# Optimization experiments

Hardware: AMD Instinct MI355X
Metric: run time of the kernel (lower is better)

Reference implementation:

```python
import jax, jax.numpy as jnp
import numpy as np

B, N = 16, 4096

def _fps(xyz, npoint):
    # iterative farthest point sampling on one cloud [n,3] -> [npoint] int32
    n = xyz.shape[0]
    def body(carry, _):
        dist, far = carry
        d = jnp.sum((xyz - xyz[far]) ** 2, axis=-1)
        dist = jnp.minimum(dist, d)
        return (dist, jnp.argmax(dist).astype(jnp.int32)), far
    _, idx = jax.lax.scan(body, (jnp.full((n,), 1e10, jnp.float32), jnp.int32(0)), None, length=npoint)
    return idx

def _ball_query(radius, nsample, xyz, new_xyz):
    # xyz [n,3], new_xyz [S,3] -> [S,nsample] neighbor indices (first-in-index order, as in PointNet++)
    n = xyz.shape[0]
    sqr = jnp.sum((new_xyz[:, None, :] - xyz[None, :, :]) ** 2, axis=-1)  # [S,n]
    idx = jnp.where(sqr > radius * radius, n, jnp.arange(n, dtype=jnp.int32)[None, :])
    idx = jnp.sort(idx, axis=-1)[:, :nsample]
    return jnp.where(idx == n, idx[:, :1], idx)

def _gather(p, i):
    return jax.vmap(lambda pp, ii: pp[ii])(p, i)

def _mlp(x, layers):
    # shared MLP = 1x1 conv over grouped points; BN(eval) folded into (W,b)
    for W, b in layers:
        x = jax.nn.relu(jnp.einsum('bsnc,co->bsno', x, W) + b)
    return x

def _sa(xyz, feats, npoint, radius, nsample, layers):
    fps_idx = jax.vmap(lambda p: _fps(p, npoint))(xyz)            # [B,S]
    new_xyz = _gather(xyz, fps_idx)                                # [B,S,3]
    idx = jax.vmap(lambda p, q: _ball_query(radius, nsample, p, q))(xyz, new_xyz)  # [B,S,ns]
    x = _gather(xyz, idx) - new_xyz[:, :, None, :]                 # centered grouped xyz
    if feats is not None:
        x = jnp.concatenate([x, _gather(feats, idx)], axis=-1)
    x = _mlp(x, layers)
    return new_xyz, jnp.max(x, axis=2)

def _forward(points, w10, b10, w11, b11, w12, b12, w20, b20, w21, b21, w22, b22, w30, b30, w31, b31, w32, b32, lw1, lb1, lw2, lb2, fw1, fb1, fw2, fb2, pos_mean, pos_std, rot_mean, rot_std):
    l1x, l1f = _sa(points, None, 512, 0.2, 32, [(w10, b10), (w11, b11), (w12, b12)])
    l2x, l2f = _sa(l1x, l1f, 128, 0.4, 64, [(w20, b20), (w21, b21), (w22, b22)])
    # sa3: group_all
    x = jnp.concatenate([l2x, l2f], axis=-1)[:, None]              # [B,1,128,259]
    x = _mlp(x, [(w30, b30), (w31, b31), (w32, b32)])
    g = jnp.max(x, axis=2).reshape(points.shape[0], 1024)
    label = jax.nn.sigmoid(jax.nn.relu(g @ lw1 + lb1) @ lw2 + lb2)  # dropout = identity (eval)
    res = jax.nn.relu(g @ fw1 + fb1) @ fw2 + fb2
    pl = res[:, 0:3] * pos_std + pos_mean
    rl = res[:, 3:9] * rot_std + rot_mean
    pr = res[:, 9:12] * pos_std + pos_mean
    rr = res[:, 12:18] * rot_std + rot_mean
    return jnp.concatenate([label, pl, rl, pr, rr], axis=-1)       # [B,20]

def setup_inputs():
    ks = iter(jax.random.split(jax.random.key(0), 64))
    def w(shape, s=0.05):
        return jax.random.normal(next(ks), shape, jnp.float32) * s
    inp = {'points': jax.random.normal(next(ks), (B, N, 3), jnp.float32) * 0.5}
    dims = {'w10': (3, 64), 'w11': (64, 64), 'w12': (64, 128), 'w20': (131, 128), 'w21': (128, 128), 'w22': (128, 256), 'w30': (259, 256), 'w31': (256, 512), 'w32': (512, 1024), 'lw1': (1024, 256), 'lw2': (256, 2), 'fw1': (1024, 512), 'fw2': (512, 18)}
    for name, s in dims.items():
        inp[name] = w(s)
        inp[name.replace('w', 'b', 1)] = jnp.zeros((s[1],), jnp.float32)
    inp['pos_mean'] = w((3,), 0.1)
    inp['pos_std'] = jnp.abs(w((3,))) + 1.0
    inp['rot_mean'] = w((6,), 0.1)
    inp['rot_std'] = jnp.abs(w((6,))) + 1.0
    return inp

def reference(points, w10, b10, w11, b11, w12, b12, w20, b20, w21, b21, w22, b22, w30, b30, w31, b31, w32, b32, lw1, lb1, lw2, lb2, fw1, fb1, fw2, fb2, pos_mean, pos_std, rot_mean, rot_std):
    return _forward(points, w10, b10, w11, b11, w12, b12, w20, b20, w21, b21, w22, b22, w30, b30, w31, b31, w32, b32, lw1, lb1, lw2, lb2, fw1, fb1, fw2, fb2, pos_mean, pos_std, rot_mean, rot_std)
```

## Files before the change

kernel.cpp:

```cpp
#include <hip/hip_runtime.h>
#include <math.h>

#define BB 16
#define NN 4096

typedef float v2f __attribute__((ext_vector_type(2)));
typedef short bfrag8 __attribute__((ext_vector_type(8)));
typedef float fx4 __attribute__((ext_vector_type(4)));

__device__ __forceinline__ v2f pkfma(v2f a, v2f b, v2f c) {
    return __builtin_elementwise_fma(a, b, c);
}

__device__ __forceinline__ fx4 mfma16(bfrag8 a, bfrag8 b, fx4 c) {
    return __builtin_amdgcn_mfma_f32_16x16x32_bf16(a, b, c, 0, 0, 0);
}

__device__ __forceinline__ unsigned short bf16rne(float v) {
    unsigned u = __float_as_uint(v);
    return (unsigned short)((u + 0x7FFFu + ((u >> 16) & 1u)) >> 16);
}
__device__ __forceinline__ void bf16split(float v, unsigned short& h, unsigned short& l) {
    h = bf16rne(v);
    float fh = __uint_as_float((unsigned)h << 16);
    l = bf16rne(v - fh);
}

__device__ __forceinline__ float sq3(float dx, float dy, float dz) {
    return __fadd_rn(__fadd_rn(__fmul_rn(dx, dx), __fmul_rn(dy, dy)), __fmul_rn(dz, dz));
}

template<int CTRL, int RMASK>
__device__ __forceinline__ unsigned long long dpp_max_step(unsigned long long P) {
    int lo = __builtin_amdgcn_update_dpp(0, (int)(unsigned)P,        CTRL, RMASK, 0xf, true);
    int hi = __builtin_amdgcn_update_dpp(0, (int)(unsigned)(P >> 32), CTRL, RMASK, 0xf, true);
    unsigned long long o = ((unsigned long long)(unsigned)hi << 32) | (unsigned)lo;
    return (o > P) ? o : P;
}

__device__ __forceinline__ unsigned long long dpp_wave_max_u64(unsigned long long P) {
    P = dpp_max_step<0x111, 0xf>(P);
    P = dpp_max_step<0x112, 0xf>(P);
    P = dpp_max_step<0x114, 0xf>(P);
    P = dpp_max_step<0x118, 0xf>(P);
    P = dpp_max_step<0x142, 0xa>(P);
    P = dpp_max_step<0x143, 0xc>(P);
    return P;
}

__device__ __forceinline__ unsigned long long u64max(unsigned long long a, unsigned long long b) {
    return (a > b) ? a : b;
}

template<int NPTS, int NPOINT, int TPB>
__global__ __launch_bounds__(TPB) void fps_kernel(const float* __restrict__ xyz,
                                                  float* __restrict__ newxyz,
                                                  float* __restrict__ out_t,
                                                  int ts) {
    constexpr int PPT = NPTS / TPB;
    constexpr int NW  = TPB / 64;
    static_assert(NPOINT <= TPB, "far-history latch needs NPOINT <= TPB");
    __shared__ float sx[NPTS], sy[NPTS], sz[NPTS];
    __shared__ __align__(16) unsigned long long slot[2][NW];
    const int b = blockIdx.x;
    const int tid = threadIdx.x;
    const float* base = xyz + (size_t)b * NPTS * 3;
    for (int i = tid; i < NPTS; i += TPB) {
        sx[i] = base[i * 3 + 0];
        sy[i] = base[i * 3 + 1];
        sz[i] = base[i * 3 + 2];
    }
    __syncthreads();
    float px[PPT], py[PPT], pz[PPT], dist[PPT];
#pragma unroll
    for (int k = 0; k < PPT; k++) {
        int p = tid + k * TPB;
        px[k] = sx[p]; py[k] = sy[p]; pz[k] = sz[p];
        dist[k] = 1e10f;
    }
    int far = 0;
    int myfar = 0;
    const int lane = tid & 63, wid = tid >> 6;
    for (int it = 0; it < NPOINT; it++) {
        if (tid == it) myfar = far;
        float fx = sx[far], fy = sy[far], fz = sz[far];
        float bv = -1.0f; int bi = 0;
#pragma unroll
        for (int k = 0; k < PPT; k++) {
            float d = sq3(px[k] - fx, py[k] - fy, pz[k] - fz);
            float nd = fminf(dist[k], d);
            dist[k] = nd;
            if (nd > bv) { bv = nd; bi = tid + k * TPB; }
        }
        unsigned long long P = ((unsigned long long)__float_as_uint(bv) << 32)
                             | (unsigned long long)(~(unsigned)bi & 0xFFFFFFFFull);
        P = dpp_wave_max_u64(P);
        int bufi = it & 1;
        if (lane == 63) slot[bufi][wid] = P;
        __syncthreads();
        unsigned long long v[NW];
#pragma unroll
        for (int w = 0; w < NW; w++) v[w] = slot[bufi][w];
#pragma unroll
        for (int st = NW / 2; st >= 1; st >>= 1)
#pragma unroll
            for (int w = 0; w < st; w++) v[w] = u64max(v[w], v[w + st]);
        far = (int)(~(unsigned)(v[0] & 0xFFFFFFFFull));
    }
    if (tid < NPOINT) {
        float fx = sx[myfar], fy = sy[myfar], fz = sz[myfar];
        newxyz[((size_t)b * NPOINT + tid) * 3 + 0] = fx;
        newxyz[((size_t)b * NPOINT + tid) * 3 + 1] = fy;
        newxyz[((size_t)b * NPOINT + tid) * 3 + 2] = fz;
        if (out_t) {
            out_t[0 * ts + b * NPOINT + tid] = fx;
            out_t[1 * ts + b * NPOINT + tid] = fy;
            out_t[2 * ts + b * NPOINT + tid] = fz;
        }
    }
}

template<int NS>
__device__ __forceinline__ void bq_body(const float* __restrict__ pts, int n,
                                        const float* __restrict__ centers, int S,
                                        float r2, int* __restrict__ outidx,
                                        int wave, int lane) {
    int b = wave / S, s = wave % S;
    const float* c = centers + ((size_t)b * S + s) * 3;
    float cx = c[0], cy = c[1], cz = c[2];
    const float* pb = pts + (size_t)b * n * 3;
    int* out = outidx + ((size_t)b * S + s) * NS;
    int total = 0, first = -1;
    int rounds = n >> 6;
    for (int r = 0; r < rounds; r++) {
        int p = (r << 6) + lane;
        float dx = pb[p * 3 + 0] - cx, dy = pb[p * 3 + 1] - cy, dz = pb[p * 3 + 2] - cz;
        float d = sq3(dx, dy, dz);
        bool pred = (d <= r2);
        unsigned long long mask = __ballot(pred);
        if (first < 0 && mask) first = (r << 6) + (__ffsll(mask) - 1);
        if (pred) {
            int rank = total + __popcll(mask & ((1ull << lane) - 1ull));
            if (rank < NS) out[rank] = p;
        }
        total += __popcll(mask);
        if (total >= NS) break;
    }
    for (int j = total + lane; j < NS; j += 64) out[j] = first;
}

__global__ __launch_bounds__(512) void bq1_fps2_kernel(const float* __restrict__ points,
                                                       const float* __restrict__ l1x,
                                                       float* __restrict__ l2x,
                                                       float* __restrict__ x3t,
                                                       int* __restrict__ idx1,
                                                       float r2a,
                                                       const float* __restrict__ w21,
                                                       const float* __restrict__ w22,
                                                       const float* __restrict__ w11s,
                                                       const float* __restrict__ w12s,
                                                       const float* __restrict__ w20s,
                                                       float* __restrict__ w21f,
                                                       float* __restrict__ w22f,
                                                       float* __restrict__ w11f,
                                                       float* __restrict__ w12f,
                                                       float* __restrict__ w20f) {
    __shared__ float sx[512], sy[512], sz[512];
    const int tid = threadIdx.x;
    const int lane = tid & 63, wid = tid >> 6;
    if (blockIdx.x < 16) {
        if (wid != 0) return;
        const int b = blockIdx.x;
        const float* base = l1x + (size_t)b * 512 * 3;
        for (int i = lane; i < 512; i += 64) {
            sx[i] = base[i * 3 + 0];
            sy[i] = base[i * 3 + 1];
            sz[i] = base[i * 3 + 2];
        }
        float px[8], py[8], pz[8], dist[8];
#pragma unroll
        for (int k = 0; k < 8; k++) {
            int p = lane + k * 64;
            px[k] = sx[p]; py[k] = sy[p]; pz[k] = sz[p];
            dist[k] = 1e10f;
        }
        int far = 0, myfar0 = 0, myfar1 = 0;
        for (int it = 0; it < 128; it++) {
            if (lane == it) myfar0 = far;
            if (lane == it - 64) myfar1 = far;
            float fx = sx[far], fy = sy[far], fz = sz[far];
            float bv = -1.0f; int bi = 0;
#pragma unroll
            for (int k = 0; k < 8; k++) {
                float d = sq3(px[k] - fx, py[k] - fy, pz[k] - fz);
                float nd = fminf(dist[k], d);
                dist[k] = nd;
                if (nd > bv) { bv = nd; bi = lane + k * 64; }
            }
            unsigned long long P = ((unsigned long long)__float_as_uint(bv) << 32)
                                 | (unsigned long long)(~(unsigned)bi & 0xFFFFFFFFull);
            P = dpp_wave_max_u64(P);
            unsigned lo = (unsigned)__builtin_amdgcn_readlane((int)(unsigned)P, 63);
            far = (int)(~lo);
        }
        {
            int s0 = lane, s1 = lane + 64;
            float a = sx[myfar0], c1 = sy[myfar0], c2 = sz[myfar0];
            l2x[((size_t)b * 128 + s0) * 3 + 0] = a;
            l2x[((size_t)b * 128 + s0) * 3 + 1] = c1;
            l2x[((size_t)b * 128 + s0) * 3 + 2] = c2;
            x3t[0 * 2048 + b * 128 + s0] = a;
            x3t[1 * 2048 + b * 128 + s0] = c1;
            x3t[2 * 2048 + b * 128 + s0] = c2;
            float d = sx[myfar1], e = sy[myfar1], f = sz[myfar1];
            l2x[((size_t)b * 128 + s1) * 3 + 0] = d;
            l2x[((size_t)b * 128 + s1) * 3 + 1] = e;
            l2x[((size_t)b * 128 + s1) * 3 + 2] = f;
            x3t[0 * 2048 + b * 128 + s1] = d;
            x3t[1 * 2048 + b * 128 + s1] = e;
            x3t[2 * 2048 + b * 128 + s1] = f;
        }
    } else if (blockIdx.x < 1040) {
        int wave = (blockIdx.x - 16) * 8 + wid;
        bq_body<32>(points, 4096, l1x, 512, r2a, idx1, wave, lane);
    } else {
        int gt = (blockIdx.x - 1040) * 512 + tid;
        const float* W; float* OF; int NT, KT, N; int t;
        if (gt < 4096)       { W = w21;        OF = w21f; NT = 8;  KT = 4; N = 128; t = gt; }
        else if (gt < 12288) { W = w22;        OF = w22f; NT = 16; KT = 4; N = 256; t = gt - 4096; }
        else if (gt < 13312) { W = w11s;       OF = w11f; NT = 4;  KT = 2; N = 64;  t = gt - 12288; }
        else if (gt < 15360) { W = w12s;       OF = w12f; NT = 8;  KT = 2; N = 128; t = gt - 13312; }
        else                 { W = w20s + 384; OF = w20f; NT = 8;  KT = 4; N = 128; t = gt - 15360; }
        int L = t & 63;
        int rest = t >> 6;
        int nt = rest & (NT - 1);
        int hk = rest / NT;
        int kt = hk % KT, hl = hk / KT;
        int k0 = kt * 32 + (L >> 4) * 8;
        int n  = nt * 16 + (L & 15);
        unsigned o[4];
#pragma unroll
        for (int e = 0; e < 4; e++) {
            float va = W[(size_t)(k0 + 2 * e + 0) * N + n];
            float vb = W[(size_t)(k0 + 2 * e + 1) * N + n];
            unsigned short ha, la, hb, lb;
            bf16split(va, ha, la);
            bf16split(vb, hb, lb);
            o[e] = hl ? ((unsigned)la | ((unsigned)lb << 16))
                      : ((unsigned)ha | ((unsigned)hb << 16));
        }
        ((uint4*)OF)[t] = make_uint4(o[0], o[1], o[2], o[3]);
    }
}

__global__ __launch_bounds__(64, 2) void sa1_bq2_kernel(const float* __restrict__ xyz, const float* __restrict__ l1x,
                                                 const int* __restrict__ idx1,
                                                 const float* __restrict__ l2x, int* __restrict__ idx2, float r2b,
                                                 const float* __restrict__ W1, const float* __restrict__ B1,
                                                 const float* __restrict__ W2f, const float* __restrict__ B2,
                                                 const float* __restrict__ W3f, const float* __restrict__ B3,
                                                 float* __restrict__ l1f) {
    __shared__ short hsh[64 * 72];
    __shared__ short hsl[64 * 72];
    int lane = threadIdx.x;
    if (blockIdx.x < 2048) {
        bq_body<64>(l1x, 512, l2x, 128, r2b, idx2, blockIdx.x, lane);
        return;
    }
    int blk = blockIdx.x - 2048;
    int b = blk >> 8;
    int ct = lane >> 5, nn = lane & 31;
    int s = ((blk & 255) << 1) | ct;
    int center = b * 512 + s;
    int c0 = b * 512 + ((blk & 255) << 1);
    int ii = idx1[center * 32 + nn];
    float px = xyz[((size_t)b * NN + ii) * 3 + 0] - l1x[(size_t)center * 3 + 0];
    float py = xyz[((size_t)b * NN + ii) * 3 + 1] - l1x[(size_t)center * 3 + 1];
    float pz = xyz[((size_t)b * NN + ii) * 3 + 2] - l1x[(size_t)center * 3 + 2];
#pragma unroll
    for (int c2 = 0; c2 < 32; c2++) {
        int ca = 2 * c2, cb = 2 * c2 + 1;
        float v0 = fmaxf(B1[ca] + px * W1[ca] + py * W1[64 + ca] + pz * W1[128 + ca], 0.0f);
        float v1 = fmaxf(B1[cb] + px * W1[cb] + py * W1[64 + cb] + pz * W1[128 + cb], 0.0f);
        unsigned short h0, l0, h1, l1;
        bf16split(v0, h0, l0);
        bf16split(v1, h1, l1);
        int base = lane * 72 + ca;
        *(unsigned*)(&hsh[base]) = (unsigned)h0 | ((unsigned)h1 << 16);
        *(unsigned*)(&hsl[base]) = (unsigned)l0 | ((unsigned)l1 << 16);
    }
    __syncthreads();
    {
        fx4 acc[4][4];
#pragma unroll
        for (int mt = 0; mt < 4; mt++)
#pragma unroll
            for (int nt = 0; nt < 4; nt++) {
                float bn = B2[nt * 16 + (lane & 15)];
                acc[mt][nt] = (fx4){bn, bn, bn, bn};
            }
        const bfrag8* w2v = (const bfrag8*)W2f;
#pragma unroll
        for (int kt = 0; kt < 2; kt++) {
            bfrag8 ah[4], al[4];
#pragma unroll
            for (int mt = 0; mt < 4; mt++) {
                int idx = (mt * 16 + (lane & 15)) * 72 + kt * 32 + (lane >> 4) * 8;
                ah[mt] = *(const bfrag8*)(&hsh[idx]);
                al[mt] = *(const bfrag8*)(&hsl[idx]);
            }
#pragma unroll
            for (int nt = 0; nt < 4; nt++) {
                bfrag8 bh = w2v[(size_t)((0 + kt) * 4 + nt) * 64 + lane];
                bfrag8 bl = w2v[(size_t)((2 + kt) * 4 + nt) * 64 + lane];
#pragma unroll
                for (int mt = 0; mt < 4; mt++) {
                    acc[mt][nt] = mfma16(ah[mt], bh, acc[mt][nt]);
                    acc[mt][nt] = mfma16(ah[mt], bl, acc[mt][nt]);
                    acc[mt][nt] = mfma16(al[mt], bh, acc[mt][nt]);
                }
            }
        }
        __syncthreads();
#pragma unroll
        for (int mt = 0; mt < 4; mt++)
#pragma unroll
            for (int nt = 0; nt < 4; nt++)
#pragma unroll
                for (int r = 0; r < 4; r++) {
                    float v = fmaxf(acc[mt][nt][r], 0.0f);
                    int m = mt * 16 + (lane >> 4) * 4 + r;
                    int n = nt * 16 + (lane & 15);
                    unsigned short hb, lb;
                    bf16split(v, hb, lb);
                    hsh[m * 72 + n] = (short)hb;
                    hsl[m * 72 + n] = (short)lb;
                }
        __syncthreads();
    }
    const bfrag8* w3v = (const bfrag8*)W3f;
#pragma unroll 1
    for (int pass = 0; pass < 2; pass++) {
        int nbase = pass * 4;
        fx4 acc[4][4];
#pragma unroll
        for (int mt = 0; mt < 4; mt++)
#pragma unroll
            for (int nt = 0; nt < 4; nt++) {
                float bn = B3[(nbase + nt) * 16 + (lane & 15)];
                acc[mt][nt] = (fx4){bn, bn, bn, bn};
            }
#pragma unroll
        for (int kt = 0; kt < 2; kt++) {
            bfrag8 ah[4], al[4];
#pragma unroll
            for (int mt = 0; mt < 4; mt++) {
                int idx = (mt * 16 + (lane & 15)) * 72 + kt * 32 + (lane >> 4) * 8;
                ah[mt] = *(const bfrag8*)(&hsh[idx]);
                al[mt] = *(const bfrag8*)(&hsl[idx]);
            }
#pragma unroll
            for (int nt = 0; nt < 4; nt++) {
                bfrag8 bh = w3v[(size_t)((0 + kt) * 8 + nbase + nt) * 64 + lane];
                bfrag8 bl = w3v[(size_t)((2 + kt) * 8 + nbase + nt) * 64 + lane];
#pragma unroll
                for (int mt = 0; mt < 4; mt++) {
                    acc[mt][nt] = mfma16(ah[mt], bh, acc[mt][nt]);
                    acc[mt][nt] = mfma16(ah[mt], bl, acc[mt][nt]);
                    acc[mt][nt] = mfma16(al[mt], bh, acc[mt][nt]);
                }
            }
        }
#pragma unroll
        for (int nt = 0; nt < 4; nt++) {
            float mv0 = 0.0f, mv1 = 0.0f;
#pragma unroll
            for (int r = 0; r < 4; r++) {
                mv0 = fmaxf(mv0, fmaxf(acc[0][nt][r], acc[1][nt][r]));
                mv1 = fmaxf(mv1, fmaxf(acc[2][nt][r], acc[3][nt][r]));
            }
            mv0 = fmaxf(mv0, __shfl_xor(mv0, 16));
            mv0 = fmaxf(mv0, __shfl_xor(mv0, 32));
            mv1 = fmaxf(mv1, __shfl_xor(mv1, 16));
            mv1 = fmaxf(mv1, __shfl_xor(mv1, 32));
            int n = (nbase + nt) * 16 + (lane & 15);
            if (lane < 16)      l1f[(size_t)c0 * 128 + n] = mv0;
            else if (lane < 32) l1f[(size_t)(c0 + 1) * 128 + n] = mv1;
        }
    }
}

__global__ __launch_bounds__(256, 4) void sa2_kernel(const float* __restrict__ l1x, const float* __restrict__ l2x,
                                                  const float* __restrict__ l1f, const int* __restrict__ idx2,
                                                  const float* __restrict__ W1, const float* __restrict__ B1,
                                                  const float* __restrict__ w20f,
                                                  const float* __restrict__ w21f, const float* __restrict__ B2,
                                                  const float* __restrict__ w22f, const float* __restrict__ B3,
                                                  float* __restrict__ x3t) {
    __shared__ short hsh[64 * 136];
    __shared__ short hsl[64 * 136];
    __shared__ float sxyz[64 * 4];
    int tid = threadIdx.x;
    int w = __builtin_amdgcn_readfirstlane(tid >> 6);
    int lane = tid & 63;
    int b = blockIdx.x >> 7, s = blockIdx.x & 127;
    int center = b * 128 + s;
    int ii = idx2[center * 64 + lane];
    float cx = l2x[(size_t)center * 3 + 0], cy = l2x[(size_t)center * 3 + 1], cz = l2x[(size_t)center * 3 + 2];
    const float* pr = l1x + ((size_t)b * 512 + ii) * 3;
    float px = pr[0] - cx, py = pr[1] - cy, pz = pr[2] - cz;
    if (w == 0) {
        sxyz[lane * 4 + 0] = px;
        sxyz[lane * 4 + 1] = py;
        sxyz[lane * 4 + 2] = pz;
    }
    {
        const float4* frow = (const float4*)(l1f + ((size_t)b * 512 + ii) * 128);
#pragma unroll
        for (int j = 0; j < 8; j++) {
            float4 f = frow[w * 8 + j];
            unsigned short h0, l0, h1, l1, h2, l2, h3, l3;
            bf16split(f.x, h0, l0);
            bf16split(f.y, h1, l1);
            bf16split(f.z, h2, l2);
            bf16split(f.w, h3, l3);
            int cb = lane * 136 + w * 32 + 4 * j;
            *(unsigned*)(&hsh[cb + 0]) = (unsigned)h0 | ((unsigned)h1 << 16);
            *(unsigned*)(&hsh[cb + 2]) = (unsigned)h2 | ((unsigned)h3 << 16);
            *(unsigned*)(&hsl[cb + 0]) = (unsigned)l0 | ((unsigned)l1 << 16);
            *(unsigned*)(&hsl[cb + 2]) = (unsigned)l2 | ((unsigned)l3 << 16);
        }
    }
    __syncthreads();
    {
        fx4 acc[4][2];
        float w0n[2], w1n[2], w2n[2];
#pragma unroll
        for (int nt = 0; nt < 2; nt++) {
            int n = (2 * w + nt) * 16 + (lane & 15);
            float bn = B1[n];
            acc[0][nt] = (fx4){bn, bn, bn, bn};
            acc[1][nt] = acc[0][nt]; acc[2][nt] = acc[0][nt]; acc[3][nt] = acc[0][nt];
            w0n[nt] = W1[n]; w1n[nt] = W1[128 + n]; w2n[nt] = W1[256 + n];
        }
#pragma unroll
        for (int mt = 0; mt < 4; mt++)
#pragma unroll
            for (int r = 0; r < 4; r++) {
                int m = mt * 16 + (lane >> 4) * 4 + r;
                float mx = sxyz[m * 4 + 0], my = sxyz[m * 4 + 1], mz = sxyz[m * 4 + 2];
#pragma unroll
                for (int nt = 0; nt < 2; nt++)
                    acc[mt][nt][r] += mx * w0n[nt] + my * w1n[nt] + mz * w2n[nt];
            }
#pragma unroll
        for (int kt = 0; kt < 4; kt++) {
            bfrag8 ah[4], al[4];
#pragma unroll
            for (int mt = 0; mt < 4; mt++) {
                int idx = (mt * 16 + (lane & 15)) * 136 + kt * 32 + (lane >> 4) * 8;
                ah[mt] = *(const bfrag8*)(&hsh[idx]);
                al[mt] = *(const bfrag8*)(&hsl[idx]);
            }
#pragma unroll
            for (int nt = 0; nt < 2; nt++) {
                int ng = 2 * w + nt;
                bfrag8 bh = ((const bfrag8*)w20f)[(size_t)((0 + kt) * 8 + ng) * 64 + lane];
                bfrag8 bl = ((const bfrag8*)w20f)[(size_t)((4 + kt) * 8 + ng) * 64 + lane];
#pragma unroll
                for (int mt = 0; mt < 4; mt++) {
                    acc[mt][nt] = mfma16(ah[mt], bh, acc[mt][nt]);
                    acc[mt][nt] = mfma16(ah[mt], bl, acc[mt][nt]);
                    acc[mt][nt] = mfma16(al[mt], bh, acc[mt][nt]);
                }
            }
        }
        __syncthreads();
#pragma unroll
        for (int mt = 0; mt < 4; mt++)
#pragma unroll
            for (int nt = 0; nt < 2; nt++)
#pragma unroll
                for (int r = 0; r < 4; r++) {
                    float v = fmaxf(acc[mt][nt][r], 0.0f);
                    int m = mt * 16 + (lane >> 4) * 4 + r;
                    int n = (2 * w + nt) * 16 + (lane & 15);
                    unsigned short hb, lb;
                    bf16split(v, hb, lb);
                    hsh[m * 136 + n] = (short)hb;
                    hsl[m * 136 + n] = (short)lb;
                }
        __syncthreads();
    }
    {
        fx4 acc[4][2];
#pragma unroll
        for (int mt = 0; mt < 4; mt++)
#pragma unroll
            for (int nt = 0; nt < 2; nt++) {
                float bn = B2[(2 * w + nt) * 16 + (lane & 15)];
                acc[mt][nt] = (fx4){bn, bn, bn, bn};
            }
#pragma unroll
        for (int kt = 0; kt < 4; kt++) {
            bfrag8 ah[4], al[4];
#pragma unroll
            for (int mt = 0; mt < 4; mt++) {
                int idx = (mt * 16 + (lane & 15)) * 136 + kt * 32 + (lane >> 4) * 8;
                ah[mt] = *(const bfrag8*)(&hsh[idx]);
                al[mt] = *(const bfrag8*)(&hsl[idx]);
            }
#pragma unroll
            for (int nt = 0; nt < 2; nt++) {
                int ng = 2 * w + nt;
                bfrag8 bh = ((const bfrag8*)w21f)[(size_t)((0 + kt) * 8 + ng) * 64 + lane];
                bfrag8 bl = ((const bfrag8*)w21f)[(size_t)((4 + kt) * 8 + ng) * 64 + lane];
#pragma unroll
                for (int mt = 0; mt < 4; mt++) {
                    acc[mt][nt] = mfma16(ah[mt], bh, acc[mt][nt]);
                    acc[mt][nt] = mfma16(ah[mt], bl, acc[mt][nt]);
                    acc[mt][nt] = mfma16(al[mt], bh, acc[mt][nt]);
                }
            }
        }
        __syncthreads();
#pragma unroll
        for (int mt = 0; mt < 4; mt++)
#pragma unroll
            for (int nt = 0; nt < 2; nt++)
#pragma unroll
                for (int r = 0; r < 4; r++) {
                    float v = fmaxf(acc[mt][nt][r], 0.0f);
                    int m = mt * 16 + (lane >> 4) * 4 + r;
                    int n = (2 * w + nt) * 16 + (lane & 15);
                    unsigned short hb, lb;
                    bf16split(v, hb, lb);
                    hsh[m * 136 + n] = (short)hb;
                    hsl[m * 136 + n] = (short)lb;
                }
        __syncthreads();
    }
#pragma unroll 1
    for (int pass = 0; pass < 2; pass++) {
        int nb = w * 4 + pass * 2;
        fx4 acc[4][2];
#pragma unroll
        for (int mt = 0; mt < 4; mt++)
#pragma unroll
            for (int nt = 0; nt < 2; nt++) {
                float bn = B3[(nb + nt) * 16 + (lane & 15)];
                acc[mt][nt] = (fx4){bn, bn, bn, bn};
            }
#pragma unroll
        for (int kt = 0; kt < 4; kt++) {
            bfrag8 ah[4], al[4];
#pragma unroll
            for (int mt = 0; mt < 4; mt++) {
                int idx = (mt * 16 + (lane & 15)) * 136 + kt * 32 + (lane >> 4) * 8;
                ah[mt] = *(const bfrag8*)(&hsh[idx]);
                al[mt] = *(const bfrag8*)(&hsl[idx]);
            }
#pragma unroll
            for (int nt = 0; nt < 2; nt++) {
                bfrag8 bh = ((const bfrag8*)w22f)[(size_t)((0 + kt) * 16 + (nb + nt)) * 64 + lane];
                bfrag8 bl = ((const bfrag8*)w22f)[(size_t)((4 + kt) * 16 + (nb + nt)) * 64 + lane];
#pragma unroll
                for (int mt = 0; mt < 4; mt++) {
                    acc[mt][nt] = mfma16(ah[mt], bh, acc[mt][nt]);
                    acc[mt][nt] = mfma16(ah[mt], bl, acc[mt][nt]);
                    acc[mt][nt] = mfma16(al[mt], bh, acc[mt][nt]);
                }
            }
        }
#pragma unroll
        for (int nt = 0; nt < 2; nt++) {
            float mv = 0.0f;
#pragma unroll
            for (int mt = 0; mt < 4; mt++)
#pragma unroll
                for (int r = 0; r < 4; r++)
                    mv = fmaxf(mv, acc[mt][nt][r]);
            mv = fmaxf(mv, __shfl_xor(mv, 16));
            mv = fmaxf(mv, __shfl_xor(mv, 32));
            if (lane < 16)
                x3t[(size_t)(3 + (nb + nt) * 16 + lane) * 2048 + center] = mv;
        }
    }
}

template<int K, int COUT, int CPT, bool MAXOUT>
__device__ __forceinline__ void gemm_t_body(const float* __restrict__ in_t,
                                            const float* __restrict__ W,
                                            const float* __restrict__ bias,
                                            float* __restrict__ outp,
                                            int bid, int lane) {
    int rw = bid & 31, cg = bid >> 5;
    int row = rw * 64 + lane;
    int cbase = cg * CPT;
    v2f acc[CPT / 2];
    const v2f* bv = (const v2f*)(bias + cbase);
#pragma unroll
    for (int j = 0; j < CPT / 2; j++) acc[j] = bv[j];
    for (int k = 0; k < K; k++) {
        float xk = in_t[(size_t)k * 2048 + row];
        v2f xk2 = {xk, xk};
        const v2f* wr = (const v2f*)(W + (size_t)k * COUT + cbase);
#pragma unroll
        for (int j = 0; j < CPT / 2; j++) acc[j] = pkfma(xk2, wr[j], acc[j]);
    }
    if (MAXOUT) {
        int b = row >> 7;
#pragma unroll
        for (int j = 0; j < CPT / 2; j++) {
            float va = fmaxf(acc[j].x, 0.0f);
            float vb = fmaxf(acc[j].y, 0.0f);
#pragma unroll
            for (int m = 32; m >= 1; m >>= 1) {
                va = fmaxf(va, __shfl_xor(va, m));
                vb = fmaxf(vb, __shfl_xor(vb, m));
            }
            if (lane == 0) {
                atomicMax((int*)(outp + (size_t)b * 1024 + cbase + 2 * j + 0), __float_as_int(va));
                atomicMax((int*)(outp + (size_t)b * 1024 + cbase + 2 * j + 1), __float_as_int(vb));
            }
        }
    } else {
#pragma unroll
        for (int j = 0; j < CPT / 2; j++) {
            outp[(size_t)(cbase + 2 * j + 0) * 2048 + row] = fmaxf(acc[j].x, 0.0f);
            outp[(size_t)(cbase + 2 * j + 1) * 2048 + row] = fmaxf(acc[j].y, 0.0f);
        }
    }
}

template<int K, int COUT, int CPT, bool MAXOUT>
__global__ __launch_bounds__(64, 4) void gemm_t_kernel(const float* __restrict__ in_t,
                                                    const float* __restrict__ W,
                                                    const float* __restrict__ bias,
                                                    float* __restrict__ outp) {
    gemm_t_body<K, COUT, CPT, MAXOUT>(in_t, W, bias, outp, blockIdx.x, threadIdx.x);
}

__global__ __launch_bounds__(64, 4) void gemm1_zerog_kernel(const float* __restrict__ in_t,
                                                            const float* __restrict__ W,
                                                            const float* __restrict__ bias,
                                                            float* __restrict__ outp,
                                                            float* __restrict__ g) {
    if (blockIdx.x < 1024) {
        gemm_t_body<259, 256, 8, false>(in_t, W, bias, outp, blockIdx.x, threadIdx.x);
    } else {
        g[(blockIdx.x - 1024) * 64 + threadIdx.x] = 0.0f;
    }
}

__global__ __launch_bounds__(512) void head_kernel(const float* __restrict__ g,
                                                   const float* __restrict__ lw1, const float* __restrict__ lb1,
                                                   const float* __restrict__ lw2, const float* __restrict__ lb2,
                                                   const float* __restrict__ fw1, const float* __restrict__ fb1,
                                                   const float* __restrict__ fw2, const float* __restrict__ fb2,
                                                   const float* __restrict__ pm, const float* __restrict__ ps,
                                                   const float* __restrict__ rm, const float* __restrict__ rs,
                                                   float* __restrict__ out) {
    __shared__ float gl[1024], a1[256], f1[512];
    int b = blockIdx.x, t = threadIdx.x;
    for (int i = t; i < 1024; i += 512) gl[i] = g[b * 1024 + i];
    __syncthreads();
    {
        float acc = fb1[t];
        for (int k = 0; k < 1024; k++) acc += gl[k] * fw1[k * 512 + t];
        f1[t] = fmaxf(acc, 0.0f);
    }
    if (t < 256) {
        float acc = lb1[t];
        for (int k = 0; k < 1024; k++) acc += gl[k] * lw1[k * 256 + t];
        a1[t] = fmaxf(acc, 0.0f);
    }
    __syncthreads();
    if (t < 2) {
        float z = lb2[t];
        for (int k = 0; k < 256; k++) z += a1[k] * lw2[k * 2 + t];
        out[b * 20 + t] = 1.0f / (1.0f + expf(-z));
    } else if (t < 20) {
        int i = t - 2;
        float z = fb2[i];
        for (int k = 0; k < 512; k++) z += f1[k] * fw2[k * 18 + i];
        float sc, mn;
        if (i < 3)       { sc = ps[i];      mn = pm[i]; }
        else if (i < 9)  { sc = rs[i - 3];  mn = rm[i - 3]; }
        else if (i < 12) { sc = ps[i - 9];  mn = pm[i - 9]; }
        else             { sc = rs[i - 12]; mn = rm[i - 12]; }
        out[b * 20 + t] = z * sc + mn;
    }
}

static inline size_t align256(size_t x) { return (x + 255) & ~(size_t)255; }

extern "C" void kernel_launch(void* const* d_in, const int* in_sizes, int n_in,
                              void* d_out, int out_size, void* d_ws, size_t ws_size,
                              hipStream_t stream) {
    const float* points = (const float*)d_in[0];
    const float* w10 = (const float*)d_in[1];  const float* b10 = (const float*)d_in[2];
    const float* w11 = (const float*)d_in[3];  const float* b11 = (const float*)d_in[4];
    const float* w12 = (const float*)d_in[5];  const float* b12 = (const float*)d_in[6];
    const float* w20 = (const float*)d_in[7];  const float* b20 = (const float*)d_in[8];
    const float* w21 = (const float*)d_in[9];  const float* b21 = (const float*)d_in[10];
    const float* w22 = (const float*)d_in[11]; const float* b22 = (const float*)d_in[12];
    const float* w30 = (const float*)d_in[13]; const float* b30 = (const float*)d_in[14];
    const float* w31 = (const float*)d_in[15]; const float* b31 = (const float*)d_in[16];
    const float* w32 = (const float*)d_in[17]; const float* b32 = (const float*)d_in[18];
    const float* lw1 = (const float*)d_in[19]; const float* lb1 = (const float*)d_in[20];
    const float* lw2 = (const float*)d_in[21]; const float* lb2 = (const float*)d_in[22];
    const float* fw1 = (const float*)d_in[23]; const float* fb1 = (const float*)d_in[24];
    const float* fw2 = (const float*)d_in[25]; const float* fb2 = (const float*)d_in[26];
    const float* pm  = (const float*)d_in[27]; const float* ps  = (const float*)d_in[28];
    const float* rm  = (const float*)d_in[29]; const float* rs  = (const float*)d_in[30];
    float* out = (float*)d_out;

    char* p = (char*)d_ws;
    float* l1x  = (float*)p; p += align256((size_t)BB * 512 * 3 * 4);
    int*   idx1 = (int*)p;   p += align256((size_t)BB * 512 * 32 * 4);
    float* l1f  = (float*)p; p += align256((size_t)BB * 512 * 128 * 4);
    float* l2x  = (float*)p; p += align256((size_t)BB * 128 * 3 * 4);
    int*   idx2 = (int*)p;   p += align256((size_t)BB * 128 * 64 * 4);
    float* x3t  = (float*)p; p += align256((size_t)259 * 2048 * 4);
    float* h1t  = (float*)p; p += align256((size_t)256 * 2048 * 4);
    float* h2t  = (float*)p; p += align256((size_t)512 * 2048 * 4);
    float* g    = (float*)p; p += align256((size_t)BB * 1024 * 4);
    float* w21f = h1t;
    float* w22f = h1t + (size_t)16384;
    float* w11f = h1t + (size_t)49152;
    float* w12f = h1t + (size_t)53248;
    float* w20f = h1t + (size_t)61440;

    const float R2A = (float)(0.2 * 0.2);
    const float R2B = (float)(0.4 * 0.4);

    fps_kernel<4096, 512, 512><<<BB, 512, 0, stream>>>(points, l1x, (float*)nullptr, 0);
    bq1_fps2_kernel<<<1078, 512, 0, stream>>>(points, l1x, l2x, x3t, idx1, R2A,
                                              w21, w22, w11, w12, w20,
                                              w21f, w22f, w11f, w12f, w20f);
    sa1_bq2_kernel<<<6144, 64, 0, stream>>>(points, l1x, idx1, l2x, idx2, R2B,
                                            w10, b10, w11f, b11, w12f, b12, l1f);
    sa2_kernel<<<2048, 256, 0, stream>>>(l1x, l2x, l1f, idx2, w20, b20,
                                         w20f, w21f, b21, w22f, b22, x3t);
    gemm1_zerog_kernel<<<1280, 64, 0, stream>>>(x3t, w30, b30, h1t, g);
    gemm_t_kernel<256, 512, 8, false><<<2048, 64, 0, stream>>>(h1t, w31, b31, h2t);
    gemm_t_kernel<512, 1024, 8, true><<<4096, 64, 0, stream>>>(h2t, w32, b32, g);
    head_kernel<<<BB, 512, 0, stream>>>(g, lw1, lb1, lw2, lb2, fw1, fb1, fw2, fb2, pm, ps, rm, rs, out);
}
```

Measured before the change: 787.3 us.

## Move SA3 MLP layers 2-3 to split-bf16 MFMA GEMMs

Replaces the scalar packed-FMA GEMMs for the 256->512 and 512->1024 SA3 layers with MFMA kernels that emulate fp32 precision using three bf16 products (hi*hi, hi*lo, lo*hi). The first GEMM now writes its activations as hi/lo bf16 pairs in row-major layout, and the extra blocks of that launch pre-split w31/w32 into fragment-ordered buffers that reuse the l1f workspace. This targets the FMA-bound cost of the large SA3 layers. In exchange it adds weight-conversion work on every call and a small precision deviation from dropping the lo*lo term.

Result: faster. 764.0 us, median of 2 (-3.0%).

```diff
diff --git a/kernel.cpp b/kernel.cpp
--- a/kernel.cpp
+++ b/kernel.cpp
@@ -147,6 +147,29 @@
         if (total >= NS) break;
     }
     for (int j = total + lane; j < NS; j += 64) out[j] = first;
+}
+
+__device__ __forceinline__ void wconv_one(const float* __restrict__ W, float* __restrict__ OF,
+                                          int NT, int KT, int N, int t) {
+    int L = t & 63;
+    int rest = t >> 6;
+    int nt = rest & (NT - 1);
+    int hk = rest / NT;
+    int kt = hk % KT, hl = hk / KT;
+    int k0 = kt * 32 + (L >> 4) * 8;
+    int n  = nt * 16 + (L & 15);
+    unsigned o[4];
+#pragma unroll
+    for (int e = 0; e < 4; e++) {
+        float va = W[(size_t)(k0 + 2 * e + 0) * N + n];
+        float vb = W[(size_t)(k0 + 2 * e + 1) * N + n];
+        unsigned short ha, la, hb, lb;
+        bf16split(va, ha, la);
+        bf16split(vb, hb, lb);
+        o[e] = hl ? ((unsigned)la | ((unsigned)lb << 16))
+                  : ((unsigned)ha | ((unsigned)hb << 16));
+    }
+    ((uint4*)OF)[t] = make_uint4(o[0], o[1], o[2], o[3]);
 }
 
 __global__ __launch_bounds__(512) void bq1_fps2_kernel(const float* __restrict__ points,
@@ -225,31 +248,11 @@
         bq_body<32>(points, 4096, l1x, 512, r2a, idx1, wave, lane);
     } else {
         int gt = (blockIdx.x - 1040) * 512 + tid;
-        const float* W; float* OF; int NT, KT, N; int t;
-        if (gt < 4096)       { W = w21;        OF = w21f; NT = 8;  KT = 4; N = 128; t = gt; }
-        else if (gt < 12288) { W = w22;        OF = w22f; NT = 16; KT = 4; N = 256; t = gt - 4096; }
-        else if (gt < 13312) { W = w11s;       OF = w11f; NT = 4;  KT = 2; N = 64;  t = gt - 12288; }
-        else if (gt < 15360) { W = w12s;       OF = w12f; NT = 8;  KT = 2; N = 128; t = gt - 13312; }
-        else                 { W = w20s + 384; OF = w20f; NT = 8;  KT = 4; N = 128; t = gt - 15360; }
-        int L = t & 63;
-        int rest = t >> 6;
-        int nt = rest & (NT - 1);
-        int hk = rest / NT;
-        int kt = hk % KT, hl = hk / KT;
-        int k0 = kt * 32 + (L >> 4) * 8;
-        int n  = nt * 16 + (L & 15);
-        unsigned o[4];
-#pragma unroll
-        for (int e = 0; e < 4; e++) {
-            float va = W[(size_t)(k0 + 2 * e + 0) * N + n];
-            float vb = W[(size_t)(k0 + 2 * e + 1) * N + n];
-            unsigned short ha, la, hb, lb;
-            bf16split(va, ha, la);
-            bf16split(vb, hb, lb);
-            o[e] = hl ? ((unsigned)la | ((unsigned)lb << 16))
-                      : ((unsigned)ha | ((unsigned)hb << 16));
-        }
-        ((uint4*)OF)[t] = make_uint4(o[0], o[1], o[2], o[3]);
+        if (gt < 4096)       wconv_one(w21,        w21f, 8,  4, 128, gt);
+        else if (gt < 12288) wconv_one(w22,        w22f, 16, 4, 256, gt - 4096);
+        else if (gt < 13312) wconv_one(w11s,       w11f, 4,  2, 64,  gt - 12288);
+        else if (gt < 15360) wconv_one(w12s,       w12f, 8,  2, 128, gt - 13312);
+        else                 wconv_one(w20s + 384, w20f, 8,  4, 128, gt - 15360);
     }
 }
 
@@ -588,12 +591,13 @@
     }
 }
 
-template<int K, int COUT, int CPT, bool MAXOUT>
-__device__ __forceinline__ void gemm_t_body(const float* __restrict__ in_t,
-                                            const float* __restrict__ W,
-                                            const float* __restrict__ bias,
-                                            float* __restrict__ outp,
-                                            int bid, int lane) {
+template<int K, int COUT, int CPT>
+__device__ __forceinline__ void gemm1_body_bf16out(const float* __restrict__ in_t,
+                                                   const float* __restrict__ W,
+                                                   const float* __restrict__ bias,
+                                                   unsigned short* __restrict__ oh,
+                                                   unsigned short* __restrict__ ol,
+                                                   int bid, int lane) {
     int rw = bid & 31, cg = bid >> 5;
     int row = rw * 64 + lane;
     int cbase = cg * CPT;
@@ -608,48 +612,117 @@
 #pragma unroll
         for (int j = 0; j < CPT / 2; j++) acc[j] = pkfma(xk2, wr[j], acc[j]);
     }
-    if (MAXOUT) {
-        int b = row >> 7;
-#pragma unroll
-        for (int j = 0; j < CPT / 2; j++) {
-            float va = fmaxf(acc[j].x, 0.0f);
-            float vb = fmaxf(acc[j].y, 0.0f);
-#pragma unroll
-            for (int m = 32; m >= 1; m >>= 1) {
-                va = fmaxf(va, __shfl_xor(va, m));
-                vb = fmaxf(vb, __shfl_xor(vb, m));
-            }
-            if (lane == 0) {
-                atomicMax((int*)(outp + (size_t)b * 1024 + cbase + 2 * j + 0), __float_as_int(va));
-                atomicMax((int*)(outp + (size_t)b * 1024 + cbase + 2 * j + 1), __float_as_int(vb));
-            }
-        }
-    } else {
-#pragma unroll
-        for (int j = 0; j < CPT / 2; j++) {
-            outp[(size_t)(cbase + 2 * j + 0) * 2048 + row] = fmaxf(acc[j].x, 0.0f);
-            outp[(size_t)(cbase + 2 * j + 1) * 2048 + row] = fmaxf(acc[j].y, 0.0f);
-        }
-    }
-}
-
-template<int K, int COUT, int CPT, bool MAXOUT>
-__global__ __launch_bounds__(64, 4) void gemm_t_kernel(const float* __restrict__ in_t,
-                                                    const float* __restrict__ W,
-                                                    const float* __restrict__ bias,
-                                                    float* __restrict__ outp) {
-    gemm_t_body<K, COUT, CPT, MAXOUT>(in_t, W, bias, outp, blockIdx.x, threadIdx.x);
+    unsigned ho[4], lo[4];
+#pragma unroll
+    for (int j = 0; j < CPT / 2; j++) {
+        float va = fmaxf(acc[j].x, 0.0f);
+        float vb = fmaxf(acc[j].y, 0.0f);
+        unsigned short ha, la, hb, lb;
+        bf16split(va, ha, la);
+        bf16split(vb, hb, lb);
+        ho[j] = (unsigned)ha | ((unsigned)hb << 16);
+        lo[j] = (unsigned)la | ((unsigned)lb << 16);
+    }
+    size_t idx = ((size_t)row * COUT + cbase) >> 3;
+    ((uint4*)oh)[idx] = make_uint4(ho[0], ho[1], ho[2], ho[3]);
+    ((uint4*)ol)[idx] = make_uint4(lo[0], lo[1], lo[2], lo[3]);
 }
 
 __global__ __launch_bounds__(64, 4) void gemm1_zerog_kernel(const float* __restrict__ in_t,
                                                             const float* __restrict__ W,
                                                             const float* __restrict__ bias,
-                                                            float* __restrict__ outp,
-                                                            float* __restrict__ g) {
+                                                            unsigned short* __restrict__ h1h,
+                                                            unsigned short* __restrict__ h1l,
+                                                            float* __restrict__ g,
+                                                            const float* __restrict__ w31,
+                                                            const float* __restrict__ w32,
+                                                            float* __restrict__ w31f,
+                                                            float* __restrict__ w32f) {
     if (blockIdx.x < 1024) {
-        gemm_t_body<259, 256, 8, false>(in_t, W, bias, outp, blockIdx.x, threadIdx.x);
+        gemm1_body_bf16out<259, 256, 8>(in_t, W, bias, h1h, h1l, blockIdx.x, threadIdx.x);
+    } else if (blockIdx.x < 1280) {
+        g[(blockIdx.x - 1024) * 64 + threadIdx.x] = 0.0f;
     } else {
-        g[(blockIdx.x - 1024) * 64 + threadIdx.x] = 0.0f;
+        int gt = (blockIdx.x - 1280) * 64 + threadIdx.x;
+        if (gt < 32768) wconv_one(w31, w31f, 32, 8,  512,  gt);
+        else            wconv_one(w32, w32f, 64, 16, 1024, gt - 32768);
+    }
+}
+
+template<int K, int NT_TOT, bool MAXOUT>
+__global__ __launch_bounds__(64, 4) void gemm_mfma_kernel(const unsigned short* __restrict__ Ah,
+                                                          const unsigned short* __restrict__ Al,
+                                                          const float* __restrict__ Wf,
+                                                          const float* __restrict__ bias,
+                                                          unsigned short* __restrict__ Oh,
+                                                          unsigned short* __restrict__ Ol,
+                                                          float* __restrict__ g) {
+    constexpr int KT = K / 32;
+    constexpr int NCOL = NT_TOT * 16;
+    int lane = threadIdx.x;
+    int mtile = blockIdx.x & 31, bn = blockIdx.x >> 5;
+    int mbase = mtile * 64;
+    int nb4 = bn * 4;
+    const bfrag8* wv = (const bfrag8*)Wf;
+    fx4 acc[4][4];
+#pragma unroll
+    for (int mt = 0; mt < 4; mt++)
+#pragma unroll
+        for (int j = 0; j < 4; j++) {
+            float bnv = bias[(nb4 + j) * 16 + (lane & 15)];
+            acc[mt][j] = (fx4){bnv, bnv, bnv, bnv};
+        }
+#pragma unroll 1
+    for (int kt = 0; kt < KT; kt++) {
+        bfrag8 ah[4], al[4];
+#pragma unroll
+        for (int mt = 0; mt < 4; mt++) {
+            size_t off = (size_t)(mbase + mt * 16 + (lane & 15)) * K + kt * 32 + (lane >> 4) * 8;
+            ah[mt] = *(const bfrag8*)(Ah + off);
+            al[mt] = *(const bfrag8*)(Al + off);
+        }
+#pragma unroll
+        for (int j = 0; j < 4; j++) {
+            bfrag8 bh = wv[(size_t)((0 * KT + kt) * NT_TOT + nb4 + j) * 64 + lane];
+            bfrag8 bl = wv[(size_t)((1 * KT + kt) * NT_TOT + nb4 + j) * 64 + lane];
+#pragma unroll
+            for (int mt = 0; mt < 4; mt++) {
+                acc[mt][j] = mfma16(ah[mt], bh, acc[mt][j]);
+                acc[mt][j] = mfma16(ah[mt], bl, acc[mt][j]);
+                acc[mt][j] = mfma16(al[mt], bh, acc[mt][j]);
+            }
+        }
+    }
+    if (MAXOUT) {
+        int b = mbase >> 7;
+#pragma unroll
+        for (int j = 0; j < 4; j++) {
+            float mv = 0.0f;
+#pragma unroll
+            for (int mt = 0; mt < 4; mt++)
+#pragma unroll
+                for (int r = 0; r < 4; r++)
+                    mv = fmaxf(mv, acc[mt][j][r]);
+            mv = fmaxf(mv, __shfl_xor(mv, 16));
+            mv = fmaxf(mv, __shfl_xor(mv, 32));
+            if (lane < 16)
+                atomicMax((int*)(g + (size_t)b * 1024 + (nb4 + j) * 16 + lane), __float_as_int(mv));
+        }
+    } else {
+#pragma unroll
+        for (int mt = 0; mt < 4; mt++)
+#pragma unroll
+            for (int j = 0; j < 4; j++)
+#pragma unroll
+                for (int r = 0; r < 4; r++) {
+                    float v = fmaxf(acc[mt][j][r], 0.0f);
+                    int m = mbase + mt * 16 + (lane >> 4) * 4 + r;
+                    int n = (nb4 + j) * 16 + (lane & 15);
+                    unsigned short hb, lb;
+                    bf16split(v, hb, lb);
+                    Oh[(size_t)m * NCOL + n] = hb;
+                    Ol[(size_t)m * NCOL + n] = lb;
+                }
     }
 }
 
@@ -731,6 +804,12 @@
     float* w11f = h1t + (size_t)49152;
     float* w12f = h1t + (size_t)53248;
     float* w20f = h1t + (size_t)61440;
+    unsigned short* h1h = (unsigned short*)h1t;
+    unsigned short* h1l = h1h + (size_t)2048 * 256;
+    unsigned short* h2h = (unsigned short*)h2t;
+    unsigned short* h2l = h2h + (size_t)2048 * 512;
+    float* w31f = l1f;
+    float* w32f = l1f + (size_t)131072;
 
     const float R2A = (float)(0.2 * 0.2);
     const float R2B = (float)(0.4 * 0.4);
@@ -743,8 +822,9 @@
                                             w10, b10, w11f, b11, w12f, b12, l1f);
     sa2_kernel<<<2048, 256, 0, stream>>>(l1x, l2x, l1f, idx2, w20, b20,
                                          w20f, w21f, b21, w22f, b22, x3t);
-    gemm1_zerog_kernel<<<1280, 64, 0, stream>>>(x3t, w30, b30, h1t, g);
-    gemm_t_kernel<256, 512, 8, false><<<2048, 64, 0, stream>>>(h1t, w31, b31, h2t);
-    gemm_t_kernel<512, 1024, 8, true><<<4096, 64, 0, stream>>>(h2t, w32, b32, g);
+    gemm1_zerog_kernel<<<3840, 64, 0, stream>>>(x3t, w30, b30, h1h, h1l, g, w31, w32, w31f, w32f);
+    gemm_mfma_kernel<256, 32, false><<<256, 64, 0, stream>>>(h1h, h1l, w31f, b31, h2h, h2l, (float*)nullptr);
+    gemm_mfma_kernel<512, 64, true><<<512, 64, 0, stream>>>(h2h, h2l, w32f, b32,
+                                                            (unsigned short*)nullptr, (unsigned short*)nullptr, g);
     head_kernel<<<BB, 512, 0, stream>>>(g, lw1, lb1, lw2, lb2, fw1, fb1, fw2, fb2, pm, ps, rm, rs, out);
 }
```
